# Performance work log

Hardware: AMD Instinct MI355X
Metric: run time of the kernel (lower is better)

The kernel has to match this reference:

```python
import jax, jax.numpy as jnp
import numpy as np

BN_EPS = 1e-5

def _bn(h, gamma, beta, mean, var):
    # inference-mode BatchNorm1d
    return (h - mean) * jax.lax.rsqrt(var + BN_EPS) * gamma + beta


def setup_inputs() -> dict:
    key = jax.random.key(0)
    ks = jax.random.split(key, 16)
    N, E, D_in, D, L = 100000, 640000, 256, 128, 3
    s = 0.05
    return {
        "x": jax.random.normal(ks[0], (N, D_in), jnp.float32),
        "edge_index": jax.random.randint(ks[1], (2, E), 0, N, jnp.int32),
        "W_in": jax.random.normal(ks[2], (D_in, D), jnp.float32) * s,
        "b_in": jax.random.normal(ks[3], (D,), jnp.float32) * s,
        "bn_in_gamma": jax.random.uniform(ks[4], (D,), jnp.float32, 0.5, 1.5),
        "bn_in_beta": jax.random.normal(ks[5], (D,), jnp.float32) * s,
        "bn_in_mean": jax.random.normal(ks[6], (D,), jnp.float32) * s,
        "bn_in_var": jax.random.uniform(ks[7], (D,), jnp.float32, 0.5, 1.5),
        "Wl": jax.random.normal(ks[8], (L, D, D), jnp.float32) * s,
        "bl": jax.random.normal(ks[9], (L, D), jnp.float32) * s,
        "Wr": jax.random.normal(ks[10], (L, D, D), jnp.float32) * s,
        "bn_gamma": jax.random.uniform(ks[11], (L, D), jnp.float32, 0.5, 1.5),
        "bn_beta": jax.random.normal(ks[12], (L, D), jnp.float32) * s,
        "bn_mean": jax.random.normal(ks[13], (L, D), jnp.float32) * s,
        "bn_var": jax.random.uniform(ks[14], (L, D), jnp.float32, 0.5, 1.5),
    }


def reference(x, edge_index, W_in, b_in, bn_in_gamma, bn_in_beta, bn_in_mean,
              bn_in_var, Wl, bl, Wr, bn_gamma, bn_beta, bn_mean, bn_var):
    N = x.shape[0]
    src, dst = edge_index[0], edge_index[1]
    # in-degree (clamped to 1 so isolated nodes aggregate to 0, matching PyG mean)
    deg = jax.ops.segment_sum(jnp.ones_like(dst, jnp.float32), dst, num_segments=N)
    deg = jnp.maximum(deg, 1.0)[:, None]  # [N, 1]

    # input projection + BN + ReLU (dropout = identity in eval)
    h = jax.nn.relu(_bn(x @ W_in + b_in, bn_in_gamma, bn_in_beta, bn_in_mean, bn_in_var))

    L = Wl.shape[0]
    for l in range(L):
        # SAGEConv(mean): lin_l(mean_j h_j) + lin_r(h_i)
        agg = jax.ops.segment_sum(h[src], dst, num_segments=N) / deg  # [N, D]
        h_new = agg @ Wl[l] + bl[l] + h @ Wr[l]
        h_new = jax.nn.relu(_bn(h_new, bn_gamma[l], bn_beta[l], bn_mean[l], bn_var[l]))
        h = h + h_new  # residual
    return h
```

## Files before the change

kernel.cpp:

```cpp
#include <hip/hip_runtime.h>

#define BN_EPS 1e-5f

typedef __bf16 bf16x8 __attribute__((ext_vector_type(8)));
typedef float f32x4 __attribute__((ext_vector_type(4)));
typedef unsigned int uint;
typedef unsigned short ushort;

__device__ __forceinline__ ushort f2bf(float f) {
  union { float f; uint u; } v; v.f = f;
  uint r = v.u + 0x7FFF + ((v.u >> 16) & 1);
  return (ushort)(r >> 16);
}
__device__ __forceinline__ float bf2f_lo(uint u) {
  union { uint i; float f; } v; v.i = u << 16; return v.f;
}
__device__ __forceinline__ float bf2f_hi(uint u) {
  union { uint i; float f; } v; v.i = u & 0xffff0000u; return v.f;
}
__device__ __forceinline__ uint pack2(float a, float b) {
  return (uint)f2bf(a) | ((uint)f2bf(b) << 16);
}


__global__ void hist_kernel(const int* __restrict__ dst, int* __restrict__ cnt, int E) {
  int e = blockIdx.x * 256 + threadIdx.x;
  if (e < E) atomicAdd(&cnt[dst[e]], 1);
}

__global__ void reserve_prep_kernel(const int* __restrict__ cnt, int* __restrict__ rowbeg,
                                    int* __restrict__ cursor,
                                    const float* __restrict__ W_in, const float* __restrict__ Wl,
                                    const float* __restrict__ Wr, ushort* __restrict__ Bfm,
                                    int NB, int N) {
  int tid = threadIdx.x;
  int b = blockIdx.x;
  if (b >= NB) {
    int p = (b - NB) * 256 + tid;
    int mat = p >> 12;
    int rem = p & 4095;
    int half = rem >> 11;
    int rem2 = rem & 2047;
    int nt = rem2 >> 8, kt2 = (rem2 >> 6) & 3, lane = rem2 & 63;
    int n = nt * 16 + (lane & 15);
    int k0 = (half * 4 + kt2) * 32 + (lane >> 4) * 8;
    ushort tmp[8];
    #pragma unroll
    for (int j = 0; j < 8; ++j) {
      int k = k0 + j;
      float v;
      if (mat == 0) v = W_in[k * 128 + n];
      else {
        int l = mat - 1;
        v = (k < 128) ? Wl[l * 16384 + k * 128 + n] : Wr[l * 16384 + (k - 128) * 128 + n];
      }
      tmp[j] = f2bf(v);
    }
    *(uint4*)&Bfm[(size_t)p * 8] = *(const uint4*)tmp;
    return;
  }
  int i = b * 256 + tid;
  int v = (i < N) ? cnt[i] : 0;
  int lane = tid & 63;
  int x = v;
  #pragma unroll
  for (int off = 1; off < 64; off <<= 1) {
    int y = __shfl_up(x, off, 64);
    if (lane >= off) x += y;
  }
  int ret = 0;
  if (lane == 63) ret = atomicAdd(cursor, x);
  int base = __shfl(ret, 63);
  if (i < N) rowbeg[i] = base + x - v;
}

__global__ void fill_kernel(const int* __restrict__ src, const int* __restrict__ dst,
                            const int* __restrict__ rowbeg, int* __restrict__ cur,
                            int* __restrict__ col, int E) {
  int e = blockIdx.x * 256 + threadIdx.x;
  if (e < E) {
    int d = dst[e];
    int p = rowbeg[d] + atomicAdd(&cur[d], 1);
    col[p] = src[e];
  }
}


template<bool F32OUT>
__global__ __launch_bounds__(256, 4)
void gemm_fused(const int* __restrict__ rowbeg, const int* __restrict__ deg,
                const int* __restrict__ col, const ushort* __restrict__ h,
                const ushort* __restrict__ Bfm, const float* __restrict__ bias,
                const float* __restrict__ gamma, const float* __restrict__ beta,
                const float* __restrict__ mean, const float* __restrict__ var,
                void* __restrict__ out, int N) {
  __shared__ __align__(16) ushort Atile[64 * 128];
  __shared__ float Cb_all[4 * 16 * 68];
  int tid = threadIdx.x;
  int m0 = blockIdx.x * 64;

  {
    int hw = tid >> 5, l32 = tid & 31;
    const ushort* hp = h + l32 * 4;
    #pragma unroll 1
    for (int i = 0; i < 8; ++i) {
      int r = hw * 8 + i;
      int node = m0 + r;
      if (node < N) {
        int beg = rowbeg[node];
        int d = deg[node];
        float di = 1.0f / (float)(d > 0 ? d : 1);
        float a0 = 0.f, a1 = 0.f, a2 = 0.f, a3 = 0.f;
        int e = beg, end = beg + d;
        for (; e + 3 < end; e += 4) {
          uint2 v0 = *(const uint2*)(hp + (size_t)col[e] * 128);
          uint2 v1 = *(const uint2*)(hp + (size_t)col[e + 1] * 128);
          uint2 v2 = *(const uint2*)(hp + (size_t)col[e + 2] * 128);
          uint2 v3 = *(const uint2*)(hp + (size_t)col[e + 3] * 128);
          a0 += (bf2f_lo(v0.x) + bf2f_lo(v1.x)) + (bf2f_lo(v2.x) + bf2f_lo(v3.x));
          a1 += (bf2f_hi(v0.x) + bf2f_hi(v1.x)) + (bf2f_hi(v2.x) + bf2f_hi(v3.x));
          a2 += (bf2f_lo(v0.y) + bf2f_lo(v1.y)) + (bf2f_lo(v2.y) + bf2f_lo(v3.y));
          a3 += (bf2f_hi(v0.y) + bf2f_hi(v1.y)) + (bf2f_hi(v2.y) + bf2f_hi(v3.y));
        }
        for (; e < end; ++e) {
          uint2 v0 = *(const uint2*)(hp + (size_t)col[e] * 128);
          a0 += bf2f_lo(v0.x); a1 += bf2f_hi(v0.x);
          a2 += bf2f_lo(v0.y); a3 += bf2f_hi(v0.y);
        }
        uint2 o;
        o.x = pack2(a0 * di, a1 * di);
        o.y = pack2(a2 * di, a3 * di);
        int widx = (r * 128 + l32 * 4) ^ ((r & 7) << 3);
        *(uint2*)&Atile[widx] = o;
      }
    }
  }
  __syncthreads();

  int wave = tid >> 6, lane = tid & 63;
  int wm = wave >> 1, wn = wave & 1, quad = lane >> 4, l16 = lane & 15;

  int rowm[2];
  #pragma unroll
  for (int mt = 0; mt < 2; ++mt) {
    int r = m0 + wm * 32 + mt * 16 + l16;
    rowm[mt] = r < N ? r : N - 1;
  }

  uint4 a_buf[2][2], b_buf[2][4];
  #pragma unroll
  for (int mt = 0; mt < 2; ++mt) {
    int lr = wm * 32 + mt * 16 + l16;
    a_buf[0][mt] = *(const uint4*)&Atile[(lr * 128 + quad * 8) ^ ((lr & 7) << 3)];
  }
  {
    const ushort* bp = Bfm + (size_t)(wn * 4 * 256 + lane) * 8;
    #pragma unroll
    for (int nt = 0; nt < 4; ++nt)
      b_buf[0][nt] = *(const uint4*)(bp + nt * 2048);
  }

  f32x4 acc[2][4] = {};

  #pragma unroll
  for (int kt = 0; kt < 8; ++kt) {
    if (kt < 7) {
      int k1 = kt + 1;
      if (k1 < 4) {
        int c = k1 * 32 + quad * 8;
        #pragma unroll
        for (int mt = 0; mt < 2; ++mt) {
          int lr = wm * 32 + mt * 16 + l16;
          a_buf[k1 & 1][mt] = *(const uint4*)&Atile[(lr * 128 + c) ^ ((lr & 7) << 3)];
        }
      } else {
        int ko = (k1 & 3) * 32 + quad * 8;
        #pragma unroll
        for (int mt = 0; mt < 2; ++mt)
          a_buf[k1 & 1][mt] = *(const uint4*)(h + (size_t)rowm[mt] * 128 + ko);
      }
      const ushort* bp = Bfm + ((size_t)(k1 >> 2) * 16384 +
                                (size_t)((wn * 4) * 256 + (k1 & 3) * 64 + lane) * 8);
      #pragma unroll
      for (int nt = 0; nt < 4; ++nt)
        b_buf[k1 & 1][nt] = *(const uint4*)(bp + nt * 2048);
    }
    __builtin_amdgcn_sched_barrier(0);
    #pragma unroll
    for (int mt = 0; mt < 2; ++mt) {
      bf16x8 af = __builtin_bit_cast(bf16x8, a_buf[kt & 1][mt]);
      #pragma unroll
      for (int nt = 0; nt < 4; ++nt)
        acc[mt][nt] = __builtin_amdgcn_mfma_f32_16x16x32_bf16(
            af, __builtin_bit_cast(bf16x8, b_buf[kt & 1][nt]), acc[mt][nt], 0, 0, 0);
    }
  }

  #pragma unroll
  for (int nt = 0; nt < 4; ++nt) {
    int c = wn * 64 + nt * 16 + l16;
    float sc = gamma[c] * rsqrtf(var[c] + BN_EPS);
    float sh = beta[c] - mean[c] * sc;
    float bi = bias[c];
    #pragma unroll
    for (int mt = 0; mt < 2; ++mt)
      #pragma unroll
      for (int r = 0; r < 4; ++r)
        acc[mt][nt][r] = fmaxf((acc[mt][nt][r] + bi) * sc + sh, 0.f);
  }

  float* Cb = Cb_all + wave * (16 * 68);
  #pragma unroll
  for (int mt = 0; mt < 2; ++mt) {
    #pragma unroll
    for (int nt = 0; nt < 4; ++nt)
      #pragma unroll
      for (int r = 0; r < 4; ++r)
        Cb[(quad * 4 + r) * 68 + nt * 16 + l16] = acc[mt][nt][r];
    #pragma unroll
    for (int i = 0; i < 4; ++i) {
      int idx = i * 64 + lane, rowl = idx >> 4, seg = idx & 15;
      int grow = m0 + wm * 32 + mt * 16 + rowl;
      if (grow < N) {
        float4 vv = *(float4*)&Cb[rowl * 68 + seg * 4];
        uint2 rv = *(const uint2*)(h + (size_t)grow * 128 + wn * 64 + seg * 4);
        vv.x += bf2f_lo(rv.x); vv.y += bf2f_hi(rv.x);
        vv.z += bf2f_lo(rv.y); vv.w += bf2f_hi(rv.y);
        if (F32OUT) {
          *(float4*)((float*)out + (size_t)grow * 128 + wn * 64 + seg * 4) = vv;
        } else {
          uint2 o;
          o.x = pack2(vv.x, vv.y); o.y = pack2(vv.z, vv.w);
          *(uint2*)((ushort*)out + (size_t)grow * 128 + wn * 64 + seg * 4) = o;
        }
      }
    }
  }
}


__global__ __launch_bounds__(256, 4)
void gemm_in(const float* __restrict__ X, const ushort* __restrict__ Bfm,
             const float* __restrict__ bias,
             const float* __restrict__ gamma, const float* __restrict__ beta,
             const float* __restrict__ mean, const float* __restrict__ var,
             ushort* __restrict__ out, int N) {
  __shared__ float Cb_all[4 * 16 * 68];
  int tid = threadIdx.x, wave = tid >> 6, lane = tid & 63;
  int wm = wave >> 1, wn = wave & 1, quad = lane >> 4, l16 = lane & 15;
  int m0 = blockIdx.x * 64;

  int rowm[2];
  #pragma unroll
  for (int mt = 0; mt < 2; ++mt) {
    int r = m0 + wm * 32 + mt * 16 + l16;
    rowm[mt] = r < N ? r : N - 1;
  }

  float4 f_buf[2][2][2];
  uint4 b_buf[2][4];
  #pragma unroll
  for (int mt = 0; mt < 2; ++mt) {
    const float* p = X + (size_t)rowm[mt] * 256 + quad * 8;
    f_buf[0][mt][0] = *(const float4*)p;
    f_buf[0][mt][1] = *(const float4*)(p + 4);
  }
  {
    const ushort* bp = Bfm + (size_t)(wn * 4 * 256 + lane) * 8;
    #pragma unroll
    for (int nt = 0; nt < 4; ++nt)
      b_buf[0][nt] = *(const uint4*)(bp + nt * 2048);
  }

  f32x4 acc[2][4] = {};

  #pragma unroll
  for (int kt = 0; kt < 8; ++kt) {
    if (kt < 7) {
      int k1 = kt + 1;
      int ko = k1 * 32 + quad * 8;
      #pragma unroll
      for (int mt = 0; mt < 2; ++mt) {
        const float* p = X + (size_t)rowm[mt] * 256 + ko;
        f_buf[k1 & 1][mt][0] = *(const float4*)p;
        f_buf[k1 & 1][mt][1] = *(const float4*)(p + 4);
      }
      const ushort* bp = Bfm + ((size_t)(k1 >> 2) * 16384 +
                                (size_t)((wn * 4) * 256 + (k1 & 3) * 64 + lane) * 8);
      #pragma unroll
      for (int nt = 0; nt < 4; ++nt)
        b_buf[k1 & 1][nt] = *(const uint4*)(bp + nt * 2048);
    }
    __builtin_amdgcn_sched_barrier(0);
    #pragma unroll
    for (int mt = 0; mt < 2; ++mt) {
      float4 lo = f_buf[kt & 1][mt][0], hi = f_buf[kt & 1][mt][1];
      uint4 av;
      av.x = pack2(lo.x, lo.y); av.y = pack2(lo.z, lo.w);
      av.z = pack2(hi.x, hi.y); av.w = pack2(hi.z, hi.w);
      bf16x8 af = __builtin_bit_cast(bf16x8, av);
      #pragma unroll
      for (int nt = 0; nt < 4; ++nt)
        acc[mt][nt] = __builtin_amdgcn_mfma_f32_16x16x32_bf16(
            af, __builtin_bit_cast(bf16x8, b_buf[kt & 1][nt]), acc[mt][nt], 0, 0, 0);
    }
  }

  #pragma unroll
  for (int nt = 0; nt < 4; ++nt) {
    int c = wn * 64 + nt * 16 + l16;
    float sc = gamma[c] * rsqrtf(var[c] + BN_EPS);
    float sh = beta[c] - mean[c] * sc;
    float bi = bias[c];
    #pragma unroll
    for (int mt = 0; mt < 2; ++mt)
      #pragma unroll
      for (int r = 0; r < 4; ++r)
        acc[mt][nt][r] = fmaxf((acc[mt][nt][r] + bi) * sc + sh, 0.f);
  }

  float* Cb = Cb_all + wave * (16 * 68);
  #pragma unroll
  for (int mt = 0; mt < 2; ++mt) {
    #pragma unroll
    for (int nt = 0; nt < 4; ++nt)
      #pragma unroll
      for (int r = 0; r < 4; ++r)
        Cb[(quad * 4 + r) * 68 + nt * 16 + l16] = acc[mt][nt][r];
    #pragma unroll
    for (int i = 0; i < 4; ++i) {
      int idx = i * 64 + lane, rowl = idx >> 4, seg = idx & 15;
      int grow = m0 + wm * 32 + mt * 16 + rowl;
      if (grow < N) {
        float4 vv = *(float4*)&Cb[rowl * 68 + seg * 4];
        uint2 o;
        o.x = pack2(vv.x, vv.y); o.y = pack2(vv.z, vv.w);
        *(uint2*)(out + (size_t)grow * 128 + wn * 64 + seg * 4) = o;
      }
    }
  }
}


extern "C" void kernel_launch(void* const* d_in, const int* in_sizes, int n_in,
                              void* d_out, int out_size, void* d_ws, size_t ws_size,
                              hipStream_t stream) {
  const float* x      = (const float*)d_in[0];
  const int*   eidx   = (const int*)d_in[1];
  const float* W_in   = (const float*)d_in[2];
  const float* b_in   = (const float*)d_in[3];
  const float* bng_in = (const float*)d_in[4];
  const float* bnb_in = (const float*)d_in[5];
  const float* bnm_in = (const float*)d_in[6];
  const float* bnv_in = (const float*)d_in[7];
  const float* Wl     = (const float*)d_in[8];
  const float* bl     = (const float*)d_in[9];
  const float* Wr     = (const float*)d_in[10];
  const float* bng    = (const float*)d_in[11];
  const float* bnb    = (const float*)d_in[12];
  const float* bnm    = (const float*)d_in[13];
  const float* bnv    = (const float*)d_in[14];

  const int N = in_sizes[0] / 256;
  const int E = in_sizes[1] / 2;
  const int NB = (N + 255) / 256;
  const int* src = eidx;
  const int* dst = eidx + E;

  char* ws = (char*)d_ws;
  size_t off = 0;
  auto alloc = [&](size_t bytes) {
    void* p = ws + off;
    off = (off + bytes + 255) & ~(size_t)255;
    return p;
  };
  int* zreg     = (int*)alloc((size_t)(2 * N + 1) * 4);
  int* cnt      = zreg;
  int* cur      = zreg + N;
  int* cursor   = zreg + 2 * N;
  int* rowbeg   = (int*)alloc((size_t)N * 4);
  int* col      = (int*)alloc((size_t)E * 4);
  ushort* Bfm   = (ushort*)alloc(4 * 32768 * 2);
  ushort* hA    = (ushort*)alloc((size_t)N * 128 * 2);
  ushort* hB    = (ushort*)alloc((size_t)N * 128 * 2);
  (void)ws_size; (void)n_in; (void)out_size;

  const int EB = (E + 255) / 256;
  const int GB = (N + 63) / 64;

  hipMemsetAsync(zreg, 0, (size_t)(2 * N + 1) * 4, stream);
  hist_kernel<<<EB, 256, 0, stream>>>(dst, cnt, E);
  reserve_prep_kernel<<<NB + 64, 256, 0, stream>>>(cnt, rowbeg, cursor,
                                                   W_in, Wl, Wr, Bfm, NB, N);
  fill_kernel<<<EB, 256, 0, stream>>>(src, dst, rowbeg, cur, col, E);

  gemm_in<<<GB, 256, 0, stream>>>(x, Bfm, b_in, bng_in, bnb_in, bnm_in, bnv_in, hA, N);

  ushort* hbuf[2] = { hA, hB };
  for (int l = 0; l < 3; ++l) {
    const ushort* h_in = hbuf[l & 1];
    const ushort* BfmL = Bfm + (size_t)(l + 1) * 32768;
    const float* biasL = bl + l * 128;
    if (l < 2) {
      gemm_fused<false><<<GB, 256, 0, stream>>>(rowbeg, cnt, col, h_in, BfmL, biasL,
          bng + l * 128, bnb + l * 128, bnm + l * 128, bnv + l * 128,
          (void*)hbuf[(l + 1) & 1], N);
    } else {
      gemm_fused<true><<<GB, 256, 0, stream>>>(rowbeg, cnt, col, h_in, BfmL, biasL,
          bng + l * 128, bnb + l * 128, bnm + l * 128, bnv + l * 128,
          d_out, N);
    }
  }
}
```

Baseline: 513.0 us.

## Split neighbor aggregation out of fused GEMM into a separate gather kernel

Moves the per-layer mean aggregation out of the fused GEMM into its own kernel, which writes a bf16 aggregate buffer. The GEMM then reads both A halves straight from global memory. The aim is to stop the gather phase (variable degree, latency-bound) from stalling the MFMA blocks and to let the gather run at its own higher occupancy with no shared tile. The cost is an extra N×128 bf16 write and read per layer plus an additional kernel launch.

```diff
diff --git a/kernel.cpp b/kernel.cpp
--- a/kernel.cpp
+++ b/kernel.cpp
@@ -86,59 +86,51 @@
 }
 
 
+__global__ void agg_kernel(const int* __restrict__ rowbeg, const int* __restrict__ deg,
+                           const int* __restrict__ col,
+                           const ushort* __restrict__ h, ushort* __restrict__ agg, int N) {
+  int node = blockIdx.x * 8 + (threadIdx.x >> 5);
+  if (node >= N) return;
+  int lane = threadIdx.x & 31;
+  const ushort* hp = h + lane * 4;
+  int beg = rowbeg[node];
+  int d = deg[node];
+  float di = 1.0f / (float)(d > 0 ? d : 1);
+  float a0 = 0.f, a1 = 0.f, a2 = 0.f, a3 = 0.f;
+  int e = beg, end = beg + d;
+  for (; e + 3 < end; e += 4) {
+    uint2 v0 = *(const uint2*)(hp + (size_t)col[e] * 128);
+    uint2 v1 = *(const uint2*)(hp + (size_t)col[e + 1] * 128);
+    uint2 v2 = *(const uint2*)(hp + (size_t)col[e + 2] * 128);
+    uint2 v3 = *(const uint2*)(hp + (size_t)col[e + 3] * 128);
+    a0 += (bf2f_lo(v0.x) + bf2f_lo(v1.x)) + (bf2f_lo(v2.x) + bf2f_lo(v3.x));
+    a1 += (bf2f_hi(v0.x) + bf2f_hi(v1.x)) + (bf2f_hi(v2.x) + bf2f_hi(v3.x));
+    a2 += (bf2f_lo(v0.y) + bf2f_lo(v1.y)) + (bf2f_lo(v2.y) + bf2f_lo(v3.y));
+    a3 += (bf2f_hi(v0.y) + bf2f_hi(v1.y)) + (bf2f_hi(v2.y) + bf2f_hi(v3.y));
+  }
+  for (; e < end; ++e) {
+    uint2 v0 = *(const uint2*)(hp + (size_t)col[e] * 128);
+    a0 += bf2f_lo(v0.x); a1 += bf2f_hi(v0.x);
+    a2 += bf2f_lo(v0.y); a3 += bf2f_hi(v0.y);
+  }
+  uint2 o;
+  o.x = pack2(a0 * di, a1 * di);
+  o.y = pack2(a2 * di, a3 * di);
+  *(uint2*)(agg + (size_t)node * 128 + lane * 4) = o;
+}
+
+
 template<bool F32OUT>
 __global__ __launch_bounds__(256, 4)
-void gemm_fused(const int* __restrict__ rowbeg, const int* __restrict__ deg,
-                const int* __restrict__ col, const ushort* __restrict__ h,
+void gemm_layer(const ushort* __restrict__ A0, const ushort* __restrict__ A1,
                 const ushort* __restrict__ Bfm, const float* __restrict__ bias,
                 const float* __restrict__ gamma, const float* __restrict__ beta,
                 const float* __restrict__ mean, const float* __restrict__ var,
-                void* __restrict__ out, int N) {
-  __shared__ __align__(16) ushort Atile[64 * 128];
+                const ushort* __restrict__ residual, void* __restrict__ out, int N) {
   __shared__ float Cb_all[4 * 16 * 68];
-  int tid = threadIdx.x;
+  int tid = threadIdx.x, wave = tid >> 6, lane = tid & 63;
+  int wm = wave >> 1, wn = wave & 1, quad = lane >> 4, l16 = lane & 15;
   int m0 = blockIdx.x * 64;
-
-  {
-    int hw = tid >> 5, l32 = tid & 31;
-    const ushort* hp = h + l32 * 4;
-    #pragma unroll 1
-    for (int i = 0; i < 8; ++i) {
-      int r = hw * 8 + i;
-      int node = m0 + r;
-      if (node < N) {
-        int beg = rowbeg[node];
-        int d = deg[node];
-        float di = 1.0f / (float)(d > 0 ? d : 1);
-        float a0 = 0.f, a1 = 0.f, a2 = 0.f, a3 = 0.f;
-        int e = beg, end = beg + d;
-        for (; e + 3 < end; e += 4) {
-          uint2 v0 = *(const uint2*)(hp + (size_t)col[e] * 128);
-          uint2 v1 = *(const uint2*)(hp + (size_t)col[e + 1] * 128);
-          uint2 v2 = *(const uint2*)(hp + (size_t)col[e + 2] * 128);
-          uint2 v3 = *(const uint2*)(hp + (size_t)col[e + 3] * 128);
-          a0 += (bf2f_lo(v0.x) + bf2f_lo(v1.x)) + (bf2f_lo(v2.x) + bf2f_lo(v3.x));
-          a1 += (bf2f_hi(v0.x) + bf2f_hi(v1.x)) + (bf2f_hi(v2.x) + bf2f_hi(v3.x));
-          a2 += (bf2f_lo(v0.y) + bf2f_lo(v1.y)) + (bf2f_lo(v2.y) + bf2f_lo(v3.y));
-          a3 += (bf2f_hi(v0.y) + bf2f_hi(v1.y)) + (bf2f_hi(v2.y) + bf2f_hi(v3.y));
-        }
-        for (; e < end; ++e) {
-          uint2 v0 = *(const uint2*)(hp + (size_t)col[e] * 128);
-          a0 += bf2f_lo(v0.x); a1 += bf2f_hi(v0.x);
-          a2 += bf2f_lo(v0.y); a3 += bf2f_hi(v0.y);
-        }
-        uint2 o;
-        o.x = pack2(a0 * di, a1 * di);
-        o.y = pack2(a2 * di, a3 * di);
-        int widx = (r * 128 + l32 * 4) ^ ((r & 7) << 3);
-        *(uint2*)&Atile[widx] = o;
-      }
-    }
-  }
-  __syncthreads();
-
-  int wave = tid >> 6, lane = tid & 63;
-  int wm = wave >> 1, wn = wave & 1, quad = lane >> 4, l16 = lane & 15;
 
   int rowm[2];
   #pragma unroll
@@ -149,10 +141,8 @@
 
   uint4 a_buf[2][2], b_buf[2][4];
   #pragma unroll
-  for (int mt = 0; mt < 2; ++mt) {
-    int lr = wm * 32 + mt * 16 + l16;
-    a_buf[0][mt] = *(const uint4*)&Atile[(lr * 128 + quad * 8) ^ ((lr & 7) << 3)];
-  }
+  for (int mt = 0; mt < 2; ++mt)
+    a_buf[0][mt] = *(const uint4*)(A0 + (size_t)rowm[mt] * 128 + quad * 8);
   {
     const ushort* bp = Bfm + (size_t)(wn * 4 * 256 + lane) * 8;
     #pragma unroll
@@ -166,19 +156,11 @@
   for (int kt = 0; kt < 8; ++kt) {
     if (kt < 7) {
       int k1 = kt + 1;
-      if (k1 < 4) {
-        int c = k1 * 32 + quad * 8;
-        #pragma unroll
-        for (int mt = 0; mt < 2; ++mt) {
-          int lr = wm * 32 + mt * 16 + l16;
-          a_buf[k1 & 1][mt] = *(const uint4*)&Atile[(lr * 128 + c) ^ ((lr & 7) << 3)];
-        }
-      } else {
-        int ko = (k1 & 3) * 32 + quad * 8;
-        #pragma unroll
-        for (int mt = 0; mt < 2; ++mt)
-          a_buf[k1 & 1][mt] = *(const uint4*)(h + (size_t)rowm[mt] * 128 + ko);
-      }
+      const ushort* bse = (k1 < 4) ? A0 : A1;
+      int ko = (k1 & 3) * 32 + quad * 8;
+      #pragma unroll
+      for (int mt = 0; mt < 2; ++mt)
+        a_buf[k1 & 1][mt] = *(const uint4*)(bse + (size_t)rowm[mt] * 128 + ko);
       const ushort* bp = Bfm + ((size_t)(k1 >> 2) * 16384 +
                                 (size_t)((wn * 4) * 256 + (k1 & 3) * 64 + lane) * 8);
       #pragma unroll
@@ -223,7 +205,7 @@
       int grow = m0 + wm * 32 + mt * 16 + rowl;
       if (grow < N) {
         float4 vv = *(float4*)&Cb[rowl * 68 + seg * 4];
-        uint2 rv = *(const uint2*)(h + (size_t)grow * 128 + wn * 64 + seg * 4);
+        uint2 rv = *(const uint2*)(residual + (size_t)grow * 128 + wn * 64 + seg * 4);
         vv.x += bf2f_lo(rv.x); vv.y += bf2f_hi(rv.x);
         vv.z += bf2f_lo(rv.y); vv.w += bf2f_hi(rv.y);
         if (F32OUT) {
@@ -383,6 +365,7 @@
   ushort* Bfm   = (ushort*)alloc(4 * 32768 * 2);
   ushort* hA    = (ushort*)alloc((size_t)N * 128 * 2);
   ushort* hB    = (ushort*)alloc((size_t)N * 128 * 2);
+  ushort* agg   = (ushort*)alloc((size_t)N * 128 * 2);
   (void)ws_size; (void)n_in; (void)out_size;
 
   const int EB = (E + 255) / 256;
@@ -399,16 +382,17 @@
   ushort* hbuf[2] = { hA, hB };
   for (int l = 0; l < 3; ++l) {
     const ushort* h_in = hbuf[l & 1];
+    agg_kernel<<<(N + 7) / 8, 256, 0, stream>>>(rowbeg, cnt, col, h_in, agg, N);
     const ushort* BfmL = Bfm + (size_t)(l + 1) * 32768;
     const float* biasL = bl + l * 128;
     if (l < 2) {
-      gemm_fused<false><<<GB, 256, 0, stream>>>(rowbeg, cnt, col, h_in, BfmL, biasL,
+      gemm_layer<false><<<GB, 256, 0, stream>>>(agg, h_in, BfmL, biasL,
           bng + l * 128, bnb + l * 128, bnm + l * 128, bnv + l * 128,
-          (void*)hbuf[(l + 1) & 1], N);
+          h_in, (void*)hbuf[(l + 1) & 1], N);
     } else {
-      gemm_fused<true><<<GB, 256, 0, stream>>>(rowbeg, cnt, col, h_in, BfmL, biasL,
+      gemm_layer<true><<<GB, 256, 0, stream>>>(agg, h_in, BfmL, biasL,
           bng + l * 128, bnb + l * 128, bnm + l * 128, bnv + l * 128,
-          d_out, N);
-    }
-  }
-}
+          h_in, d_out, N);
+    }
+  }
+}
```

Measured after the change: 468.0 us. 1.1x faster.
